# Performance work log

Hardware: AMD Instinct MI355X
Metric: run time of the kernel (lower is better)

The kernel has to match this reference:

```python
import jax, jax.numpy as jnp
import numpy as np

B, S, DIM = 2, 2048, 2048
N_HEADS, N_KV_HEADS, HEAD_DIM = 16, 4, 128
ROPE_THETA = 10000.0
N_REP = N_HEADS // N_KV_HEADS


def make_freq_cis(seq_len, head_dim, theta):
    # (seq_len, head_dim//2, 2, 2) rotation matrices [[cos,-sin],[sin,cos]]
    freqs = 1.0 / (theta ** (np.arange(0, head_dim, 2, dtype=np.float32) / head_dim))
    t = np.arange(seq_len, dtype=np.float32)
    ang = np.outer(t, freqs)  # [S, head_dim//2]
    cos, sin = np.cos(ang), np.sin(ang)
    row0 = np.stack([cos, -sin], axis=-1)
    row1 = np.stack([sin, cos], axis=-1)
    return jnp.asarray(np.stack([row0, row1], axis=-2))  # [S, hd/2, 2, 2]


def setup_inputs() -> dict:
    key = jax.random.key(0)
    ks = jax.random.split(key, 5)
    std = DIM ** -0.5
    x = jax.random.normal(ks[0], (B, S, DIM), dtype=jnp.float32)
    wq = jax.random.normal(ks[1], (N_HEADS * HEAD_DIM, DIM), dtype=jnp.float32) * std
    wk = jax.random.normal(ks[2], (N_KV_HEADS * HEAD_DIM, DIM), dtype=jnp.float32) * std
    wv = jax.random.normal(ks[3], (N_KV_HEADS * HEAD_DIM, DIM), dtype=jnp.float32) * std
    wo = jax.random.normal(ks[4], (DIM, N_HEADS * HEAD_DIM), dtype=jnp.float32) * std
    freq_cis = make_freq_cis(S, HEAD_DIM, ROPE_THETA)
    return {"x": x, "freq_cis": freq_cis, "wq": wq, "wk": wk, "wv": wv, "wo": wo}


def apply_rotary(xh, fc):
    # xh: [B,S,H,hd]; fc: [S, hd/2, 2, 2]
    b, s, h, hd = xh.shape
    xr = xh.reshape(b, s, h, hd // 2, 2)
    out = jnp.einsum('bshdj,sdij->bshdi', xr, fc)
    return out.reshape(b, s, h, hd)


def attention_fwd(x, freq_cis, wq, wk, wv, wo):
    b, s, _ = x.shape
    xq = (x @ wq.T).reshape(b, s, N_HEADS, HEAD_DIM)
    xk = (x @ wk.T).reshape(b, s, N_KV_HEADS, HEAD_DIM)
    xv = (x @ wv.T).reshape(b, s, N_KV_HEADS, HEAD_DIM)
    xq = apply_rotary(xq, freq_cis[:s])
    xk = apply_rotary(xk, freq_cis[:s])
    # GQA repeat_kv (repeat_interleave along head dim)
    xk = jnp.repeat(xk, N_REP, axis=2)
    xv = jnp.repeat(xv, N_REP, axis=2)
    scale = HEAD_DIM ** -0.5
    scores = jnp.einsum('bqhd,bkhd->bhqk', xq, xk) * scale
    causal = jnp.tril(jnp.ones((s, s), dtype=bool))
    scores = jnp.where(causal[None, None], scores, jnp.float32(-1e30))
    probs = jax.nn.softmax(scores, axis=-1)
    out = jnp.einsum('bhqk,bkhd->bqhd', probs, xv).reshape(b, s, N_HEADS * HEAD_DIM)
    return out @ wo.T


def reference(x, freq_cis, wq, wk, wv, wo):
    return attention_fwd(x, freq_cis, wq, wk, wv, wo)
```

## Files before the change

### kernel.cpp

```cpp
#include <hip/hip_runtime.h>

#define S_LEN 2048
#define N_B 2
#define N_H 16
#define N_KVH 4
#define HD 128
#define LDQ 2048
#define LDK 1024

typedef __bf16 bf16x8 __attribute__((ext_vector_type(8)));
typedef float f32x4 __attribute__((ext_vector_type(4)));
typedef float f32x16 __attribute__((ext_vector_type(16)));
typedef int v2i __attribute__((ext_vector_type(2)));

__device__ __forceinline__ float bf2f(unsigned short u){
  unsigned int x = ((unsigned int)u) << 16; float f;
  __builtin_memcpy(&f, &x, 4); return f;
}
__device__ __forceinline__ unsigned short f2bf(float f){
  unsigned int x; __builtin_memcpy(&x, &f, 4);
  unsigned int r = x + 0x7fff + ((x >> 16) & 1);
  return (unsigned short)(r >> 16);
}
__device__ __forceinline__ unsigned int cvt_pk_bf16(float lo, float hi){
  unsigned int u;
  asm("v_cvt_pk_bf16_f32 %0, %1, %2" : "=v"(u) : "v"(lo), "v"(hi));
  return u;
}
__device__ __forceinline__ void gload16(const void* g, void* l){
  __builtin_amdgcn_global_load_lds((const __attribute__((address_space(1))) void*)g,
                                   (__attribute__((address_space(3))) void*)l, 16, 0, 0);
}

__global__ void cast_bf16(const float* __restrict__ in, unsigned short* __restrict__ out, int n8){
  int i = blockIdx.x * 256 + threadIdx.x;
  if (i >= n8) return;
  const float4* p = (const float4*)in + (size_t)i * 2;
  float4 a = p[0], b = p[1];
  uint4 o;
  o.x = (unsigned)f2bf(a.x) | ((unsigned)f2bf(a.y) << 16);
  o.y = (unsigned)f2bf(a.z) | ((unsigned)f2bf(a.w) << 16);
  o.z = (unsigned)f2bf(b.x) | ((unsigned)f2bf(b.y) << 16);
  o.w = (unsigned)f2bf(b.z) | ((unsigned)f2bf(b.w) << 16);
  ((uint4*)out)[i] = o;
}

__global__ void rope_kernel(unsigned short* __restrict__ X, const float* __restrict__ FC,
                            int cpr_log2, int ld_log2, int n8){
  int i = blockIdx.x * 256 + threadIdx.x;
  if (i >= n8) return;
  int row = i >> cpr_log2;
  int col = (i & ((1 << cpr_log2) - 1)) << 3;
  size_t idx = ((size_t)row << ld_log2) + col;
  int s = row & (S_LEN - 1);
  int d = col & (HD - 1);
  uint4 v = *(const uint4*)(X + idx);
  unsigned short* pv = (unsigned short*)&v;
  const float4* f4 = (const float4*)FC + ((size_t)s * 64 + (d >> 1));
  uint4 ov; unsigned short* po = (unsigned short*)&ov;
#pragma unroll
  for (int p = 0; p < 4; p++){
    float4 f = f4[p];
    float e = bf2f(pv[2*p]), o = bf2f(pv[2*p+1]);
    po[2*p]   = f2bf(f.x * e + f.y * o);
    po[2*p+1] = f2bf(f.z * e + f.w * o);
  }
  *(uint4*)(X + idx) = ov;
}

__global__ void transpose_v(const unsigned short* __restrict__ V, unsigned short* __restrict__ Vt, int ld){
  __shared__ unsigned short tile[32][33];
  int t = threadIdx.x;
  int s0 = blockIdx.x * 32;
  int c0 = blockIdx.y * 32;
  int r = t >> 3, cg = (t & 7) * 4;
  uint2 in2 = *(const uint2*)(V + (size_t)(s0 + r) * ld + c0 + cg);
  unsigned short* pi = (unsigned short*)&in2;
  tile[r][cg+0] = pi[0]; tile[r][cg+1] = pi[1]; tile[r][cg+2] = pi[2]; tile[r][cg+3] = pi[3];
  __syncthreads();
  int b = s0 >> 11, sl = s0 & (S_LEN - 1);
  int kvh = c0 >> 7, dd0 = c0 & (HD - 1);
  int dd = t >> 3, sg = (t & 7) * 4;
  uint2 o2; unsigned short* po = (unsigned short*)&o2;
  po[0] = tile[sg+0][dd]; po[1] = tile[sg+1][dd]; po[2] = tile[sg+2][dd]; po[3] = tile[sg+3][dd];
  *(uint2*)(Vt + (size_t)((b * N_KVH + kvh) * HD + dd0 + dd) * S_LEN + sl + sg) = o2;
}

__device__ __forceinline__ void storeC(float* C, size_t idx, float v){ C[idx] = v; }
__device__ __forceinline__ void storeC(unsigned short* C, size_t idx, float v){ C[idx] = f2bf(v); }

template <typename OutT>
__global__ __launch_bounds__(256, 2) void gemm_nt(const unsigned short* __restrict__ A,
                                                  const unsigned short* __restrict__ Bm,
                                                  OutT* __restrict__ C,
                                                  int M, int N, int K, int nbn){
  extern __shared__ char smem[];
  char* sA = smem; char* sB = smem + 16384;
  int bid = blockIdx.x;
  int bn = bid % nbn, bm = bid / nbn;
  int row0 = bm * 128, col0 = bn * 128;
  int t = threadIdx.x; int w = t >> 6, l = t & 63;
  int lr = l & 15, lg = l >> 4;
  int srow = t >> 3;
  int sg = (t & 7) ^ (srow & 7);
  const unsigned short* agp = A + (size_t)(row0 + srow) * K + sg * 8;
  const unsigned short* bgp = Bm + (size_t)(col0 + srow) * K + sg * 8;
  int wr = w >> 1, wc = w & 1;
  f32x4 acc[4][4] = {};
  for (int k0 = 0; k0 < K; k0 += 64){
    __syncthreads();
#pragma unroll
    for (int i = 0; i < 4; i++){
      gload16(agp + (size_t)i * 32 * K + k0, sA + i * 4096 + w * 1024);
      gload16(bgp + (size_t)i * 32 * K + k0, sB + i * 4096 + w * 1024);
    }
    __syncthreads();
#pragma unroll
    for (int kk = 0; kk < 2; kk++){
      bf16x8 af[4], bfv[4];
#pragma unroll
      for (int m = 0; m < 4; m++){
        int row = wr * 64 + m * 16 + lr;
        int kg = kk * 4 + lg;
        af[m] = *(const bf16x8*)(sA + row * 128 + ((kg ^ (row & 7)) << 4));
      }
#pragma unroll
      for (int n = 0; n < 4; n++){
        int row = wc * 64 + n * 16 + lr;
        int kg = kk * 4 + lg;
        bfv[n] = *(const bf16x8*)(sB + row * 128 + ((kg ^ (row & 7)) << 4));
      }
#pragma unroll
      for (int m = 0; m < 4; m++)
#pragma unroll
        for (int n = 0; n < 4; n++)
          acc[m][n] = __builtin_amdgcn_mfma_f32_16x16x32_bf16(af[m], bfv[n], acc[m][n], 0, 0, 0);
    }
  }
#pragma unroll
  for (int m = 0; m < 4; m++)
#pragma unroll
    for (int n = 0; n < 4; n++)
#pragma unroll
      for (int r = 0; r < 4; r++){
        int rr = row0 + wr * 64 + m * 16 + lg * 4 + r;
        int cc = col0 + wc * 64 + n * 16 + lr;
        storeC(C, (size_t)rr * N + cc, acc[m][n][r]);
      }
}

__global__ __launch_bounds__(256, 2) void attn_fwd(const unsigned short* __restrict__ Q,
                                                   const unsigned short* __restrict__ Kb,
                                                   const unsigned short* __restrict__ Vt,
                                                   unsigned short* __restrict__ P0,
                                                   unsigned short* __restrict__ P1,
                                                   float2* __restrict__ ML){
  extern __shared__ char smem[];
  const float SOFT_C = 0.088388347648318447f * 1.4426950408889634f;
  const float THR_RAW = 62.0f;
  int bid = blockIdx.x;
  int slot = bid & 15, h = (bid >> 4) & 15, b = bid >> 8;
  int p = slot & 7, half = slot >> 3;
  int kvh = h >> 2;
  int t = threadIdx.x, w = t >> 6, l = t & 63;
  int lq = l & 31, lh = l >> 5;
  unsigned short* Pout = half ? P1 : P0;
  float2* mlb = ML + half * (N_B * S_LEN * N_H);

  int gA = (t & 15) ^ (t >> 4);
  const unsigned short* kgp = Kb + ((size_t)(b * S_LEN) + (t >> 4)) * LDK + kvh * HD + gA * 8;
  int gV = (t & 7) ^ ((t >> 3) & 7);
  const unsigned short* vgp = Vt + ((size_t)((b * N_KVH + kvh) * HD) + (t >> 3)) * S_LEN + gV * 8;

  for (int phase = 0; phase < 2; phase++){
    int qt = phase ? (15 - p) : p;
    int q_lane = qt * 128 + w * 32 + lq;
    const unsigned short* qbase = Q + ((size_t)(b * S_LEN + q_lane)) * LDQ + h * HD + lh * 8;
    bf16x8 qf[8];
#pragma unroll
    for (int ks = 0; ks < 8; ks++)
      qf[ks] = *(const bf16x8*)(qbase + ks * 16);

    f32x16 o_acc[4] = {};
    float m_run = -1e4f, l_run = 0.f;
    int t_begin = half ? (qt + 1) : 0;
    int t_end   = half ? (2 * qt + 2) : (qt + 1);

    int pk0 = t_begin * 64;
#pragma unroll
    for (int m = 0; m < 4; m++)
      gload16(kgp + (size_t)(pk0 + m * 16) * LDK, smem + m * 4096 + w * 1024);
#pragma unroll
    for (int i = 0; i < 4; i++)
      gload16(vgp + (size_t)i * 32 * S_LEN + pk0, smem + 16384 + i * 4096 + w * 1024);
    __syncthreads();

    int cur = 0;
    for (int tix = t_begin; tix < t_end; tix++){
      int k0 = tix * 64;
      char* sK = smem + (cur << 15);
      char* sV = sK + 16384;
      if (tix + 1 < t_end){
        char* nb = smem + ((cur ^ 1) << 15);
        int nk0 = k0 + 64;
#pragma unroll
        for (int m = 0; m < 4; m++)
          gload16(kgp + (size_t)(nk0 + m * 16) * LDK, nb + m * 4096 + w * 1024);
#pragma unroll
        for (int i = 0; i < 4; i++)
          gload16(vgp + (size_t)i * 32 * S_LEN + nk0, nb + 16384 + i * 4096 + w * 1024);
      }

      f32x16 sc[2] = {};
      __builtin_amdgcn_s_setprio(1);
#pragma unroll
      for (int ks = 0; ks < 8; ks++){
#pragma unroll
        for (int n = 0; n < 2; n++){
          int row = n * 32 + lq;
          int pg = (ks * 2 + lh) ^ (row & 15);
          bf16x8 kf = *(const bf16x8*)(sK + row * 256 + pg * 16);
          sc[n] = __builtin_amdgcn_mfma_f32_32x32x16_bf16(kf, qf[ks], sc[n], 0, 0, 0);
        }
      }
      __builtin_amdgcn_s_setprio(0);
      if (tix >= 2 * qt){
#pragma unroll
        for (int n = 0; n < 2; n++)
#pragma unroll
          for (int reg = 0; reg < 16; reg++){
            int kv = k0 + n * 32 + (reg & 3) + 8 * (reg >> 2) + 4 * lh;
            if (kv > q_lane) sc[n][reg] = -1e30f;
          }
      }
      float tmax = sc[0][0];
#pragma unroll
      for (int n = 0; n < 2; n++)
#pragma unroll
        for (int reg = 0; reg < 16; reg++) tmax = fmaxf(tmax, sc[n][reg]);
      tmax = fmaxf(tmax, __shfl_xor(tmax, 32));
      if (!__all(tmax - m_run <= THR_RAW)){
        float nm = fmaxf(m_run, tmax);
        float rs = exp2f((m_run - nm) * SOFT_C);
        m_run = nm;
        l_run *= rs;
#pragma unroll
        for (int n = 0; n < 4; n++)
#pragma unroll
          for (int j = 0; j < 16; j++) o_acc[n][j] *= rs;
      }
      float lsum = 0.f;
#pragma unroll
      for (int n = 0; n < 2; n++)
#pragma unroll
        for (int reg = 0; reg < 16; reg++){
          float pv = exp2f((sc[n][reg] - m_run) * SOFT_C);
          sc[n][reg] = pv;
          lsum += pv;
        }
      lsum += __shfl_xor(lsum, 32);
      l_run += lsum;

      bf16x8 pb[4];
#pragma unroll
      for (int ks = 0; ks < 4; ks++){
        int n = ks >> 1;
        int R0 = (2 * ks) & 3, R1 = (2 * ks + 1) & 3;
        unsigned int WA0 = cvt_pk_bf16(sc[n][4 * R0 + 0], sc[n][4 * R0 + 1]);
        unsigned int WA1 = cvt_pk_bf16(sc[n][4 * R0 + 2], sc[n][4 * R0 + 3]);
        unsigned int WB0 = cvt_pk_bf16(sc[n][4 * R1 + 0], sc[n][4 * R1 + 1]);
        unsigned int WB1 = cvt_pk_bf16(sc[n][4 * R1 + 2], sc[n][4 * R1 + 3]);
        v2i s0 = __builtin_amdgcn_permlane32_swap((int)WA0, (int)WB0, false, false);
        v2i s1 = __builtin_amdgcn_permlane32_swap((int)WA1, (int)WB1, false, false);
        unsigned int pu[4] = {(unsigned int)s0.x, (unsigned int)s1.x,
                              (unsigned int)s0.y, (unsigned int)s1.y};
        pb[ks] = *(bf16x8*)pu;
      }
      __builtin_amdgcn_s_setprio(1);
#pragma unroll
      for (int n = 0; n < 4; n++){
#pragma unroll
        for (int ks = 0; ks < 4; ks++){
          int row = n * 32 + lq;
          int pg = (ks * 2 + lh) ^ (row & 7);
          bf16x8 vf = *(const bf16x8*)(sV + row * 128 + pg * 16);
          o_acc[n] = __builtin_amdgcn_mfma_f32_32x32x16_bf16(vf, pb[ks], o_acc[n], 0, 0, 0);
        }
      }
      __builtin_amdgcn_s_setprio(0);
      __syncthreads();
      cur ^= 1;
    }
    unsigned short* ob = Pout + ((size_t)(b * S_LEN + q_lane)) * LDQ + h * HD + 4 * lh;
#pragma unroll
    for (int n = 0; n < 4; n++)
#pragma unroll
      for (int g = 0; g < 4; g++){
        unsigned int u0 = cvt_pk_bf16(o_acc[n][4 * g + 0], o_acc[n][4 * g + 1]);
        unsigned int u1 = cvt_pk_bf16(o_acc[n][4 * g + 2], o_acc[n][4 * g + 3]);
        uint2 o2; o2.x = u0; o2.y = u1;
        *(uint2*)(ob + n * 32 + g * 8) = o2;
      }
    if (lh == 0)
      mlb[(size_t)(b * S_LEN + q_lane) * N_H + h] = make_float2(m_run, l_run);
  }
}

__global__ void attn_merge(unsigned short* __restrict__ P0, const unsigned short* __restrict__ P1,
                           const float2* __restrict__ ML){
  const float SOFT_C = 0.088388347648318447f * 1.4426950408889634f;
  int tid = blockIdx.x * 256 + threadIdx.x;
  float2 a = ML[tid >> 4];
  float2 c = ML[(N_B * S_LEN * N_H) + (tid >> 4)];
  float m = fmaxf(a.x, c.x);
  float w0 = exp2f((a.x - m) * SOFT_C) * a.y;
  float w1 = exp2f((c.x - m) * SOFT_C) * c.y;
  float inv = 1.0f / (w0 + w1);
  float s0 = exp2f((a.x - m) * SOFT_C) * inv;
  float s1 = exp2f((c.x - m) * SOFT_C) * inv;
  uint4 u0 = *(const uint4*)(P0 + (size_t)tid * 8);
  uint4 u1 = *(const uint4*)(P1 + (size_t)tid * 8);
  unsigned short* q0 = (unsigned short*)&u0;
  unsigned short* q1 = (unsigned short*)&u1;
  uint4 o;
  unsigned int* po = (unsigned int*)&o;
#pragma unroll
  for (int j = 0; j < 4; j++){
    float lo = s0 * bf2f(q0[2*j])   + s1 * bf2f(q1[2*j]);
    float hi = s0 * bf2f(q0[2*j+1]) + s1 * bf2f(q1[2*j+1]);
    po[j] = cvt_pk_bf16(lo, hi);
  }
  *(uint4*)(P0 + (size_t)tid * 8) = o;
}

extern "C" void kernel_launch(void* const* d_in, const int* in_sizes, int n_in,
                              void* d_out, int out_size, void* d_ws, size_t ws_size,
                              hipStream_t stream) {
  const float* x  = (const float*)d_in[0];
  const float* fc = (const float*)d_in[1];
  const float* wq = (const float*)d_in[2];
  const float* wk = (const float*)d_in[3];
  const float* wv = (const float*)d_in[4];
  const float* wo = (const float*)d_in[5];
  float* out = (float*)d_out;

  char* ws = (char*)d_ws;
  unsigned short* xb  = (unsigned short*)(ws);
  unsigned short* wqb = (unsigned short*)(ws + 16777216);
  unsigned short* wkb = (unsigned short*)(ws + 25165824);
  unsigned short* wvb = (unsigned short*)(ws + 27262976);
  unsigned short* wob = (unsigned short*)(ws + 29360128);
  unsigned short* qb_ = (unsigned short*)(ws + 37748736);
  unsigned short* kvb = (unsigned short*)(ws + 54525952);
  unsigned short* vtb = (unsigned short*)(ws + 62914560);
  unsigned short* ab_ = (unsigned short*)(ws + 67108864);
  unsigned short* p1_ = xb;
  float2*         ml_ = (float2*)wqb;

  cast_bf16<<<4096, 256, 0, stream>>>(x,  xb,  1048576);
  cast_bf16<<<2048, 256, 0, stream>>>(wq, wqb, 524288);
  cast_bf16<<<512,  256, 0, stream>>>(wk, wkb, 131072);
  cast_bf16<<<512,  256, 0, stream>>>(wv, wvb, 131072);
  cast_bf16<<<2048, 256, 0, stream>>>(wo, wob, 524288);

  gemm_nt<unsigned short><<<512, 256, 32768, stream>>>(xb, wqb, qb_, 4096, 2048, 2048, 16);
  gemm_nt<unsigned short><<<256, 256, 32768, stream>>>(xb, wkb, kvb, 4096, 1024, 2048, 8);

  rope_kernel<<<4096, 256, 0, stream>>>(qb_, fc, 8, 11, 1048576);
  rope_kernel<<<1024, 256, 0, stream>>>(kvb, fc, 6, 10, 262144);

  transpose_v<<<dim3(128, 16), 256, 0, stream>>>(kvb + 512, vtb, 1024);

  attn_fwd<<<512, 256, 65536, stream>>>(qb_, kvb, vtb, ab_, p1_, ml_);
  attn_merge<<<4096, 256, 0, stream>>>(ab_, p1_, ml_);

  gemm_nt<float><<<512, 256, 32768, stream>>>(ab_, wob, out, 4096, 2048, 2048, 16);
}
```

Measured before the change: 223.3 us.

## Add triple-buffered 128x256 GEMM and XCD-aware block remapping

```diff
diff --git a/kernel.cpp b/kernel.cpp
--- a/kernel.cpp
+++ b/kernel.cpp
@@ -97,6 +97,7 @@
   extern __shared__ char smem[];
   char* sA = smem; char* sB = smem + 16384;
   int bid = blockIdx.x;
+  bid = (bid & 7) * (gridDim.x >> 3) + (bid >> 3);
   int bn = bid % nbn, bm = bid / nbn;
   int row0 = bm * 128, col0 = bn * 128;
   int t = threadIdx.x; int w = t >> 6, l = t & 63;
@@ -149,6 +150,91 @@
       }
 }
 
+template <typename OutT>
+__global__ __launch_bounds__(512, 2) void gemm_tpl(const unsigned short* __restrict__ A,
+                                                   const unsigned short* __restrict__ Bm,
+                                                   OutT* __restrict__ C,
+                                                   int M, int N, int K, int nbn){
+  extern __shared__ char smem[];
+  int bid = blockIdx.x;
+  bid = (bid & 7) * (gridDim.x >> 3) + (bid >> 3);
+  int bn = bid % nbn, bm = bid / nbn;
+  int row0 = bm * 128, col0 = bn * 256;
+  int t = threadIdx.x, w = t >> 6, l = t & 63;
+  int lr = l & 15, lg = l >> 4;
+  int wm = w >> 2, wn = w & 3;
+  int srow = t >> 3;
+  int sg = (t & 7) ^ (srow & 7);
+  const unsigned short* agp = A + (size_t)(row0 + srow) * K + sg * 8;
+  const unsigned short* bgp = Bm + (size_t)(col0 + srow) * K + sg * 8;
+  int nk = K >> 6;
+  f32x4 acc[4][4] = {};
+
+#define TPL_STAGE(j, s) do {                                                   \
+    char* base_ = smem + (s) * 49152;                                          \
+    int k0_ = (j) << 6;                                                        \
+    _Pragma("unroll")                                                          \
+    for (int i_ = 0; i_ < 2; i_++)                                             \
+      gload16(agp + (size_t)i_ * 64 * K + k0_, base_ + i_ * 8192 + w * 1024);  \
+    _Pragma("unroll")                                                          \
+    for (int i_ = 0; i_ < 4; i_++)                                             \
+      gload16(bgp + (size_t)i_ * 64 * K + k0_, base_ + 16384 + i_ * 8192 + w * 1024); \
+  } while(0)
+
+  TPL_STAGE(0, 0);
+  TPL_STAGE(1, 1);
+  int slot = 0;
+  for (int j = 0; j < nk; j++){
+    if (j + 1 < nk) asm volatile("s_waitcnt vmcnt(6)" ::: "memory");
+    else            asm volatile("s_waitcnt vmcnt(0)" ::: "memory");
+    __builtin_amdgcn_s_barrier();
+    asm volatile("" ::: "memory");
+    char* sA = smem + slot * 49152;
+    char* sB = sA + 16384;
+    bf16x8 af[2][4], bf[2][4];
+#pragma unroll
+    for (int kk = 0; kk < 2; kk++){
+#pragma unroll
+      for (int m = 0; m < 4; m++){
+        int row = wm * 64 + m * 16 + lr;
+        int kg = kk * 4 + lg;
+        af[kk][m] = *(const bf16x8*)(sA + row * 128 + ((kg ^ (row & 7)) << 4));
+      }
+#pragma unroll
+      for (int n = 0; n < 4; n++){
+        int row = wn * 64 + n * 16 + lr;
+        int kg = kk * 4 + lg;
+        bf[kk][n] = *(const bf16x8*)(sB + row * 128 + ((kg ^ (row & 7)) << 4));
+      }
+    }
+    if (j + 2 < nk){
+      int sn = slot + 2; if (sn >= 3) sn -= 3;
+      TPL_STAGE(j + 2, sn);
+    }
+    __builtin_amdgcn_s_setprio(1);
+#pragma unroll
+    for (int kk = 0; kk < 2; kk++)
+#pragma unroll
+      for (int m = 0; m < 4; m++)
+#pragma unroll
+        for (int n = 0; n < 4; n++)
+          acc[m][n] = __builtin_amdgcn_mfma_f32_16x16x32_bf16(af[kk][m], bf[kk][n], acc[m][n], 0, 0, 0);
+    __builtin_amdgcn_s_setprio(0);
+    slot++; if (slot == 3) slot = 0;
+  }
+#undef TPL_STAGE
+#pragma unroll
+  for (int m = 0; m < 4; m++)
+#pragma unroll
+    for (int n = 0; n < 4; n++)
+#pragma unroll
+      for (int r = 0; r < 4; r++){
+        int rr = row0 + wm * 64 + m * 16 + lg * 4 + r;
+        int cc = col0 + wn * 64 + n * 16 + lr;
+        storeC(C, (size_t)rr * N + cc, acc[m][n][r]);
+      }
+}
+
 __global__ __launch_bounds__(256, 2) void attn_fwd(const unsigned short* __restrict__ Q,
                                                    const unsigned short* __restrict__ Kb,
                                                    const unsigned short* __restrict__ Vt,
@@ -159,6 +245,7 @@
   const float SOFT_C = 0.088388347648318447f * 1.4426950408889634f;
   const float THR_RAW = 62.0f;
   int bid = blockIdx.x;
+  bid = ((bid & 7) << 6) | (bid >> 3);
   int slot = bid & 15, h = (bid >> 4) & 15, b = bid >> 8;
   int p = slot & 7, half = slot >> 3;
   int kvh = h >> 2;
@@ -363,7 +450,7 @@
   cast_bf16<<<512,  256, 0, stream>>>(wv, wvb, 131072);
   cast_bf16<<<2048, 256, 0, stream>>>(wo, wob, 524288);
 
-  gemm_nt<unsigned short><<<512, 256, 32768, stream>>>(xb, wqb, qb_, 4096, 2048, 2048, 16);
+  gemm_tpl<unsigned short><<<256, 512, 147456, stream>>>(xb, wqb, qb_, 4096, 2048, 2048, 8);
   gemm_nt<unsigned short><<<256, 256, 32768, stream>>>(xb, wkb, kvb, 4096, 1024, 2048, 8);
 
   rope_kernel<<<4096, 256, 0, stream>>>(qb_, fc, 8, 11, 1048576);
@@ -374,5 +461,5 @@
   attn_fwd<<<512, 256, 65536, stream>>>(qb_, kvb, vtb, ab_, p1_, ml_);
   attn_merge<<<4096, 256, 0, stream>>>(ab_, p1_, ml_);
 
-  gemm_nt<float><<<512, 256, 32768, stream>>>(ab_, wob, out, 4096, 2048, 2048, 16);
-}
+  gemm_tpl<float><<<256, 512, 147456, stream>>>(ab_, wob, out, 4096, 2048, 2048, 8);
+}
```

Result: faster. 213.5 us (-4.4%).
